# Optimization experiments

Measured on AMD Instinct MI355X. Metric: run time of the kernel, lower is better.

Reference implementation:

```python
import jax, jax.numpy as jnp
import numpy as np

B, L, D, DI, DS, DC, DTR = 128, 31, 1024, 2048, 16, 5, 64

def setup_inputs() -> dict:
    key = jax.random.key(0)
    ks = jax.random.split(key, 12)
    rn = lambda k, shp, s=0.02: jax.random.normal(k, shp, dtype=jnp.float32) * s
    return {
        "x": jax.random.normal(ks[0], (B, L, D), dtype=jnp.float32),
        "norm1_w": jnp.ones((D,), jnp.float32), "norm1_b": jnp.zeros((D,), jnp.float32),
        "in_proj_W": rn(ks[1], (2 * DI, D)),
        "conv_w": rn(ks[2], (DI, DC), 0.2), "conv_b": jnp.zeros((DI,), jnp.float32),
        "x_proj_W": rn(ks[3], (DTR + 2 * DS, DI)),
        "dt_proj_W": rn(ks[4], (DI, DTR), 0.1),
        "dt_proj_b": jnp.full((DI,), -4.6, dtype=jnp.float32),  # softplus^-1(~0.01)
        "A_log": jnp.tile(jnp.log(jnp.arange(1, DS + 1, dtype=jnp.float32))[None, :], (DI, 1)),
        "D_ssm": jnp.ones((DI,), jnp.float32),
        "out_proj_W": rn(ks[5], (D, DI)),
        "norm2_w": jnp.ones((D,), jnp.float32), "norm2_b": jnp.zeros((D,), jnp.float32),
        "ffn_W1": rn(ks[6], (2 * D, D)), "ffn_b1": jnp.zeros((2 * D,), jnp.float32),
        "ffn_W2": rn(ks[7], (D, 2 * D)), "ffn_b2": jnp.zeros((D,), jnp.float32),
        "cls_W1": rn(ks[8], (D, L * D)), "cls_b1": jnp.zeros((D,), jnp.float32),
        "cls_W2": rn(ks[9], (1, D)), "cls_b2": jnp.zeros((1,), jnp.float32),
    }

def _ln(x, w, b):
    m = x.mean(-1, keepdims=True)
    v = x.var(-1, keepdims=True)
    return (x - m) * jax.lax.rsqrt(v + 1e-5) * w + b

def _mamba(x, in_proj_W, conv_w, conv_b, x_proj_W, dt_proj_W, dt_proj_b, A_log, D_ssm, out_proj_W):
    # in_proj -> (u, z)
    xz = jnp.einsum('bld,ed->ble', x, in_proj_W)            # (B,L,2*DI)
    u, z = jnp.split(xz, 2, axis=-1)
    # causal depthwise conv1d (kernel DC) + SiLU
    xp = jnp.pad(u, ((0, 0), (DC - 1, 0), (0, 0)))
    uc = conv_b + sum(xp[:, k:k + L, :] * conv_w[:, k] for k in range(DC))
    uc = jax.nn.silu(uc)
    # input-dependent dt, B, C
    x_dbl = jnp.einsum('bld,ed->ble', uc, x_proj_W)         # (B,L,DTR+2*DS)
    dt, Bm, Cm = jnp.split(x_dbl, [DTR, DTR + DS], axis=-1)
    dt = jax.nn.softplus(jnp.einsum('blr,dr->bld', dt, dt_proj_W) + dt_proj_b)
    A = -jnp.exp(A_log)                                      # (DI,DS)
    def step(h, ins):
        dt_t, B_t, C_t, u_t = ins                            # (B,DI),(B,DS),(B,DS),(B,DI)
        dA = jnp.exp(dt_t[:, :, None] * A)                   # (B,DI,DS)
        h = h * dA + dt_t[:, :, None] * B_t[:, None, :] * u_t[:, :, None]
        y = jnp.einsum('bds,bs->bd', h, C_t)
        return h, y
    h0 = jnp.zeros((u.shape[0], DI, DS), u.dtype)
    _, ys = jax.lax.scan(step, h0, (dt.transpose(1, 0, 2), Bm.transpose(1, 0, 2),
                                    Cm.transpose(1, 0, 2), uc.transpose(1, 0, 2)))
    y = ys.transpose(1, 0, 2) + uc * D_ssm                   # skip term D*u
    y = y * jax.nn.silu(z)                                   # gate
    return jnp.einsum('bld,ed->ble', y, out_proj_W)

def reference(x, norm1_w, norm1_b, in_proj_W, conv_w, conv_b, x_proj_W, dt_proj_W,
              dt_proj_b, A_log, D_ssm, out_proj_W, norm2_w, norm2_b, ffn_W1, ffn_b1,
              ffn_W2, ffn_b2, cls_W1, cls_b1, cls_W2, cls_b2):
    # single encoder block (n_layers=1), dropout = identity (eval)
    res = x
    h = _ln(x, norm1_w, norm1_b)
    h = _mamba(h, in_proj_W, conv_w, conv_b, x_proj_W, dt_proj_W, dt_proj_b,
               A_log, D_ssm, out_proj_W)
    x = res + h
    res = x
    h = _ln(x, norm2_w, norm2_b)
    h = jax.nn.silu(jnp.einsum('bld,ed->ble', h, ffn_W1) + ffn_b1)
    h = jnp.einsum('ble,de->bld', h, ffn_W2) + ffn_b2
    x = res + h
    # classifier: Flatten -> Linear -> SiLU -> Linear
    flat = x.reshape(x.shape[0], -1)                          # (B, L*D)
    c = jax.nn.silu(flat @ cls_W1.T + cls_b1)
    out = c @ cls_W2.T + cls_b2                               # (B,1)
    return (out, x)
```

## Files before the change

### kernel.cpp

```cpp
#include <hip/hip_runtime.h>
#include <cstddef>
#include <cstdint>

#define B_   128
#define L_   31
#define D_   1024
#define DI_  2048
#define DS_  16
#define DC_  5
#define DTR_ 64
#define ROWS (B_ * L_)
#define MPAD 4096
#define KCLS (L_ * D_)

#define W_IN  0
#define W_OUT 4194304
#define W_F1  6291456
#define W_F2  8388608
#define W_XP  10485760
#define W_DT  10747904
#define WTOT  10878976

typedef unsigned short u16;
typedef __attribute__((ext_vector_type(8))) short s16x8;
typedef __attribute__((ext_vector_type(4))) float f32x4;

__device__ __forceinline__ float silu_f(float x) { return x / (1.0f + __expf(-x)); }

__device__ __forceinline__ u16 f2b(float f) {
    union { float f; uint32_t u; } c; c.f = f;
    uint32_t u = c.u + 0x7FFF + ((c.u >> 16) & 1);
    return (u16)(u >> 16);
}
__device__ __forceinline__ float b2f(u16 b) {
    union { uint32_t u; float f; } c; c.u = ((uint32_t)b) << 16;
    return c.f;
}
__device__ __forceinline__ uint32_t pack2(float lo, float hi) {
    return (uint32_t)f2b(lo) | ((uint32_t)f2b(hi) << 16);
}
__device__ __forceinline__ void cvt8(const float* __restrict__ s, u16* __restrict__ d) {
    const float4* p = (const float4*)s;
    float4 a = p[0], b = p[1];
    uint4 r;
    r.x = pack2(a.x, a.y); r.y = pack2(a.z, a.w);
    r.z = pack2(b.x, b.y); r.w = pack2(b.z, b.w);
    *(uint4*)d = r;
}

#define GLD16(g, s) __builtin_amdgcn_global_load_lds( \
    (const __attribute__((address_space(1))) void*)(g), \
    (__attribute__((address_space(3))) void*)(s), 16, 0, 0)

__global__ __launch_bounds__(256) void f2b_all_kernel(
    const float* __restrict__ inW, const float* __restrict__ outW,
    const float* __restrict__ f1W, const float* __restrict__ f2W,
    const float* __restrict__ xpW, const float* __restrict__ dtW,
    u16* __restrict__ wbuf)
{
    int g = blockIdx.x * 256 + threadIdx.x;
    if (g < 524288) { cvt8(inW + (size_t)g * 8, wbuf + W_IN + (size_t)g * 8); return; }
    g -= 524288;
    if (g < 262144) { cvt8(outW + (size_t)g * 8, wbuf + W_OUT + (size_t)g * 8); return; }
    g -= 262144;
    if (g < 262144) { cvt8(f1W + (size_t)g * 8, wbuf + W_F1 + (size_t)g * 8); return; }
    g -= 262144;
    if (g < 262144) { cvt8(f2W + (size_t)g * 8, wbuf + W_F2 + (size_t)g * 8); return; }
    g -= 262144;
    if (g < 32768) {
        const int row = g >> 8, col8 = (g & 255) * 8;
        u16* d = wbuf + W_XP + (size_t)row * 2048 + col8;
        if (row < 96) cvt8(xpW + (size_t)row * 2048 + col8, d);
        else *(uint4*)d = make_uint4(0, 0, 0, 0);
        return;
    }
    g -= 32768;
    if (g < 16384) cvt8(dtW + (size_t)g * 8, wbuf + W_DT + (size_t)g * 8);
}

__global__ __launch_bounds__(256) void ln_kernel(const float* __restrict__ x,
                                                 const float* __restrict__ w,
                                                 const float* __restrict__ b,
                                                 u16* __restrict__ y)
{
    const int row = blockIdx.x;
    const float* xr = x + (size_t)row * D_;
    float v[4];
    float sum = 0.f, sq = 0.f;
#pragma unroll
    for (int i = 0; i < 4; i++) {
        v[i] = xr[threadIdx.x + i * 256];
        sum += v[i];
        sq  += v[i] * v[i];
    }
#pragma unroll
    for (int o = 32; o > 0; o >>= 1) {
        sum += __shfl_down(sum, o, 64);
        sq  += __shfl_down(sq, o, 64);
    }
    __shared__ float red[8];
    const int wid = threadIdx.x >> 6;
    if ((threadIdx.x & 63) == 0) { red[wid] = sum; red[4 + wid] = sq; }
    __syncthreads();
    sum = red[0] + red[1] + red[2] + red[3];
    sq  = red[4] + red[5] + red[6] + red[7];
    const float mean = sum * (1.0f / D_);
    const float var  = sq * (1.0f / D_) - mean * mean;
    const float rstd = rsqrtf(var + 1e-5f);
    u16* yr = y + (size_t)row * D_;
#pragma unroll
    for (int i = 0; i < 4; i++) {
        const int c = threadIdx.x + i * 256;
        yr[c] = f2b((v[i] - mean) * rstd * w[c] + b[c]);
    }
}

__global__ __launch_bounds__(256) void ln2_fuse_kernel(const float* __restrict__ x,
                                                       const float* __restrict__ pq,
                                                       const float* __restrict__ w,
                                                       const float* __restrict__ b,
                                                       float* __restrict__ x2,
                                                       u16* __restrict__ y)
{
    const int row = blockIdx.x;
    const size_t base = (size_t)row * D_;
    const size_t PS = (size_t)ROWS * D_;
    float v[4];
    float sum = 0.f, sq = 0.f;
#pragma unroll
    for (int i = 0; i < 4; i++) {
        const int c = threadIdx.x + i * 256;
        float s = x[base + c];
        s += pq[base + c];
        s += pq[PS + base + c];
        s += pq[2 * PS + base + c];
        s += pq[3 * PS + base + c];
        x2[base + c] = s;
        v[i] = s;
        sum += s;
        sq  += s * s;
    }
#pragma unroll
    for (int o = 32; o > 0; o >>= 1) {
        sum += __shfl_down(sum, o, 64);
        sq  += __shfl_down(sq, o, 64);
    }
    __shared__ float red[8];
    const int wid = threadIdx.x >> 6;
    if ((threadIdx.x & 63) == 0) { red[wid] = sum; red[4 + wid] = sq; }
    __syncthreads();
    sum = red[0] + red[1] + red[2] + red[3];
    sq  = red[4] + red[5] + red[6] + red[7];
    const float mean = sum * (1.0f / D_);
    const float var  = sq * (1.0f / D_) - mean * mean;
    const float rstd = rsqrtf(var + 1e-5f);
    u16* yr = y + base;
#pragma unroll
    for (int i = 0; i < 4; i++) {
        const int c = threadIdx.x + i * 256;
        yr[c] = f2b((v[i] - mean) * rstd * w[c] + b[c]);
    }
}

__global__ __launch_bounds__(256) void add4_bias_kernel(const float* __restrict__ x2,
                                                        const float* __restrict__ pq,
                                                        const float* __restrict__ b2,
                                                        float* __restrict__ x3)
{
    const int i = blockIdx.x * 256 + threadIdx.x;
    const size_t PS4 = (size_t)ROWS * D_ / 4;
    float4 a  = ((const float4*)x2)[i];
    float4 c0 = ((const float4*)pq)[i];
    float4 c1 = ((const float4*)pq)[PS4 + i];
    float4 c2 = ((const float4*)pq)[2 * PS4 + i];
    float4 c3 = ((const float4*)pq)[3 * PS4 + i];
    float4 bb = ((const float4*)b2)[i & 255];
    float4 r;
    r.x = a.x + c0.x + c1.x + c2.x + c3.x + bb.x;
    r.y = a.y + c0.y + c1.y + c2.y + c3.y + bb.y;
    r.z = a.z + c0.z + c1.z + c2.z + c3.z + bb.z;
    r.w = a.w + c0.w + c1.w + c2.w + c3.w + bb.w;
    ((float4*)x3)[i] = r;
}

template <int ACT, bool BIAS, int OUT>
__global__ __launch_bounds__(512, 2) void gemm256(
    const u16* __restrict__ A, const u16* __restrict__ W,
    const float* __restrict__ bias, void* __restrict__ Cout,
    int K, int Nout, int kLen)
{
    __shared__ __align__(16) u16 As[2][256 * 64];
    __shared__ __align__(16) u16 Bs[2][256 * 64];
    const int tid = threadIdx.x;
    const int l = tid & 63;
    const int w = tid >> 6, wr = w >> 2, wc = w & 3;
    const int lane15 = l & 15, lhi = l >> 4;
    const int key = lane15 & 7;
    const int bm = blockIdx.y * 256, bn = blockIdx.x * 256;
    const int kOff = blockIdx.z * kLen;

    const int srow = tid >> 3;
    const int sg   = tid & 7;
    const int sgx  = sg ^ (srow & 7);
    const u16* gA = A + (size_t)(bm + srow) * K + kOff + sgx * 8;
    const u16* gB = W + (size_t)(bn + srow) * K + kOff + sgx * 8;
    const int soff = srow * 64 + sg * 8;

    const int NT = kLen / 64;
    f32x4 acc[8][4] = {};

#pragma unroll
    for (int c = 0; c < 4; c++) {
        GLD16(gA + (size_t)c * 64 * K, &As[0][c * 4096 + soff]);
        GLD16(gB + (size_t)c * 64 * K, &Bs[0][c * 4096 + soff]);
    }
    __syncthreads();

    for (int t = 0; t < NT; t++) {
        const int cur = t & 1;
        if (t + 1 < NT) {
            const size_t go = (size_t)(t + 1) * 64;
#pragma unroll
            for (int c = 0; c < 4; c++) {
                GLD16(gA + (size_t)c * 64 * K + go, &As[cur ^ 1][c * 4096 + soff]);
                GLD16(gB + (size_t)c * 64 * K + go, &Bs[cur ^ 1][c * 4096 + soff]);
            }
        }
        const u16* as = As[cur];
        const u16* bs = Bs[cur];
        s16x8 bf[2][4];
#pragma unroll
        for (int ks = 0; ks < 2; ks++)
#pragma unroll
            for (int ni = 0; ni < 4; ni++)
                bf[ks][ni] = *(const s16x8*)(bs + (wc * 64 + ni * 16 + lane15) * 64
                                                + (((ks * 4 + lhi) ^ key)) * 8);
#pragma unroll
        for (int mh = 0; mh < 2; mh++) {
            s16x8 af[2][4];
#pragma unroll
            for (int ks = 0; ks < 2; ks++)
#pragma unroll
                for (int mi = 0; mi < 4; mi++)
                    af[ks][mi] = *(const s16x8*)(as + (wr * 128 + mh * 64 + mi * 16 + lane15) * 64
                                                    + (((ks * 4 + lhi) ^ key)) * 8);
#pragma unroll
            for (int ks = 0; ks < 2; ks++)
#pragma unroll
                for (int mi = 0; mi < 4; mi++)
#pragma unroll
                    for (int ni = 0; ni < 4; ni++)
                        acc[mh * 4 + mi][ni] = __builtin_amdgcn_mfma_f32_16x16x32_bf16(
                            af[ks][mi], bf[ks][ni], acc[mh * 4 + mi][ni], 0, 0, 0);
        }
        __syncthreads();
    }

#pragma unroll
    for (int ni = 0; ni < 4; ni++) {
        const int col = bn + wc * 64 + ni * 16 + lane15;
        const float bv = BIAS ? bias[col] : 0.0f;
#pragma unroll
        for (int mi8 = 0; mi8 < 8; mi8++) {
#pragma unroll
            for (int r = 0; r < 4; r++) {
                const int row = bm + wr * 128 + mi8 * 16 + lhi * 4 + r;
                if (row >= ROWS) continue;
                float v = acc[mi8][ni][r] + bv;
                if (ACT == 1) v = silu_f(v);
                if (OUT == 1) ((u16*)Cout)[(size_t)row * Nout + col] = f2b(v);
                else          ((float*)Cout)[((size_t)blockIdx.z * ROWS + row) * Nout + col] = v;
            }
        }
    }
}

template <int ACT, bool BIAS, int OUT>
__global__ __launch_bounds__(256) void gemm_mfma(
    const u16* __restrict__ A, const u16* __restrict__ W,
    const float* __restrict__ bias, void* __restrict__ Cout,
    int M, int K, int Nout, int kLen)
{
    __shared__ __align__(16) u16 As[128 * 32];
    __shared__ __align__(16) u16 Bs[128 * 32];
    const int tid = threadIdx.x;
    const int l = tid & 63, w = tid >> 6;
    const int bm = blockIdx.y * 128, bn = blockIdx.x * 128;
    const int kOff = blockIdx.z * kLen;

    const int sr = l >> 2;
    const int sk = (l & 3) * 8;
    const u16* gA = A + (size_t)(bm + w * 16 + sr) * K + kOff + sk;
    const u16* gB = W + (size_t)(bn + w * 16 + sr) * K + kOff + sk;
    u16* lA = As + (w * 16 + sr) * 32 + sk;
    u16* lB = Bs + (w * 16 + sr) * 32 + sk;

    const int lane15 = l & 15, lhi = l >> 4;
    const int wr = w >> 1, wc = w & 1;
    const u16* fA = As + (wr * 64 + lane15) * 32 + lhi * 8;
    const u16* fB = Bs + (wc * 64 + lane15) * 32 + lhi * 8;

    f32x4 acc[4][4] = {};

    for (int kk = 0; kk < kLen; kk += 32) {
        GLD16(gA, lA); GLD16(gA + (size_t)64 * K, lA + 64 * 32);
        GLD16(gB, lB); GLD16(gB + (size_t)64 * K, lB + 64 * 32);
        gA += 32; gB += 32;
        __syncthreads();
        s16x8 af[4], bfr[4];
#pragma unroll
        for (int mi = 0; mi < 4; mi++) af[mi]  = *(const s16x8*)(fA + mi * 16 * 32);
#pragma unroll
        for (int ni = 0; ni < 4; ni++) bfr[ni] = *(const s16x8*)(fB + ni * 16 * 32);
#pragma unroll
        for (int mi = 0; mi < 4; mi++)
#pragma unroll
            for (int ni = 0; ni < 4; ni++)
                acc[mi][ni] = __builtin_amdgcn_mfma_f32_16x16x32_bf16(
                    af[mi], bfr[ni], acc[mi][ni], 0, 0, 0);
        __syncthreads();
    }

#pragma unroll
    for (int ni = 0; ni < 4; ni++) {
        const int col = bn + wc * 64 + ni * 16 + lane15;
        if (col >= Nout) continue;
        const float bv = BIAS ? bias[col] : 0.0f;
#pragma unroll
        for (int mi = 0; mi < 4; mi++) {
#pragma unroll
            for (int r = 0; r < 4; r++) {
                const int row = bm + wr * 64 + mi * 16 + lhi * 4 + r;
                float v = acc[mi][ni][r] + bv;
                if (ACT == 2) v = (v > 20.0f) ? v : log1pf(__expf(v));
                if (OUT == 1) ((u16*)Cout)[(size_t)row * Nout + col] = f2b(v);
                if (OUT == 2) atomicAdd(&((float*)Cout)[(size_t)row * Nout + col], v);
            }
        }
    }
}

#define KCH 512
__global__ __launch_bounds__(256) void gemm_cls_mfma(
    const float* __restrict__ A, const float* __restrict__ W,
    float* __restrict__ C)
{
    __shared__ __align__(16) u16 As[128 * 32];
    __shared__ __align__(16) u16 Bs[128 * 32];
    const int tid = threadIdx.x;
    const int l = tid & 63, w = tid >> 6;
    const int bn = blockIdx.x * 128;
    const int k0 = blockIdx.y * KCH;

    const int sr = l >> 2;
    const int sk = (l & 3) * 8;
    const int row = w * 16 + sr;
    const float* gA0 = A + (size_t)row * KCLS + k0 + sk;
    const float* gA1 = gA0 + (size_t)64 * KCLS;
    const float* gB0 = W + (size_t)(bn + row) * KCLS + k0 + sk;
    const float* gB1 = gB0 + (size_t)64 * KCLS;
    u16* lA0 = As + row * 32 + sk;  u16* lA1 = lA0 + 64 * 32;
    u16* lB0 = Bs + row * 32 + sk;  u16* lB1 = lB0 + 64 * 32;

    const int lane15 = l & 15, lhi = l >> 4;
    const int wr = w >> 1, wc = w & 1;
    const u16* fA = As + (wr * 64 + lane15) * 32 + lhi * 8;
    const u16* fB = Bs + (wc * 64 + lane15) * 32 + lhi * 8;

    f32x4 acc[4][4] = {};

    for (int ks = 0; ks < KCH / 32; ks++) {
        float4 a00 = *(const float4*)(gA0);     float4 a01 = *(const float4*)(gA0 + 4);
        float4 a10 = *(const float4*)(gA1);     float4 a11 = *(const float4*)(gA1 + 4);
        float4 b00 = *(const float4*)(gB0);     float4 b01 = *(const float4*)(gB0 + 4);
        float4 b10 = *(const float4*)(gB1);     float4 b11 = *(const float4*)(gB1 + 4);
        gA0 += 32; gA1 += 32; gB0 += 32; gB1 += 32;
        __syncthreads();
        uint4 r;
        r.x = pack2(a00.x, a00.y); r.y = pack2(a00.z, a00.w);
        r.z = pack2(a01.x, a01.y); r.w = pack2(a01.z, a01.w);
        *(uint4*)lA0 = r;
        r.x = pack2(a10.x, a10.y); r.y = pack2(a10.z, a10.w);
        r.z = pack2(a11.x, a11.y); r.w = pack2(a11.z, a11.w);
        *(uint4*)lA1 = r;
        r.x = pack2(b00.x, b00.y); r.y = pack2(b00.z, b00.w);
        r.z = pack2(b01.x, b01.y); r.w = pack2(b01.z, b01.w);
        *(uint4*)lB0 = r;
        r.x = pack2(b10.x, b10.y); r.y = pack2(b10.z, b10.w);
        r.z = pack2(b11.x, b11.y); r.w = pack2(b11.z, b11.w);
        *(uint4*)lB1 = r;
        __syncthreads();
        s16x8 af[4], bfr[4];
#pragma unroll
        for (int mi = 0; mi < 4; mi++) af[mi]  = *(const s16x8*)(fA + mi * 16 * 32);
#pragma unroll
        for (int ni = 0; ni < 4; ni++) bfr[ni] = *(const s16x8*)(fB + ni * 16 * 32);
#pragma unroll
        for (int mi = 0; mi < 4; mi++)
#pragma unroll
            for (int ni = 0; ni < 4; ni++)
                acc[mi][ni] = __builtin_amdgcn_mfma_f32_16x16x32_bf16(
                    af[mi], bfr[ni], acc[mi][ni], 0, 0, 0);
    }

#pragma unroll
    for (int ni = 0; ni < 4; ni++) {
        const int col = bn + wc * 64 + ni * 16 + lane15;
#pragma unroll
        for (int mi = 0; mi < 4; mi++) {
#pragma unroll
            for (int r = 0; r < 4; r++) {
                const int m = wr * 64 + mi * 16 + lhi * 4 + r;
                atomicAdd(&C[(size_t)m * 1024 + col], acc[mi][ni][r]);
            }
        }
    }
}

__global__ __launch_bounds__(256) void conv_silu_kernel(const u16* __restrict__ xz,
                                                        const float* __restrict__ cw,
                                                        const float* __restrict__ cb,
                                                        u16* __restrict__ uc)
{
    const int idx = blockIdx.x * 256 + threadIdx.x;
    const int d  = idx & (DI_ - 1);
    const int bl = idx >> 11;
    const int l  = bl % L_;
    const int b  = bl / L_;
    const u16* u = xz + (size_t)b * L_ * (2 * DI_) + d;
    float acc = cb[d];
#pragma unroll
    for (int k = 0; k < DC_; k++) {
        const int ll = l + k - (DC_ - 1);
        if (ll >= 0) acc = fmaf(b2f(u[(size_t)ll * (2 * DI_)]), cw[d * DC_ + k], acc);
    }
    uc[(size_t)bl * DI_ + d] = f2b(silu_f(acc));
}

__global__ __launch_bounds__(256) void dtext_kernel(const float* __restrict__ xdbl,
                                                    u16* __restrict__ dtb)
{
    const int idx = blockIdx.x * 256 + threadIdx.x;
    const int row = idx >> 4, c4 = (idx & 15) * 4;
    float4 v = *(const float4*)(xdbl + (size_t)row * 96 + c4);
    uint2 r;
    r.x = pack2(v.x, v.y); r.y = pack2(v.z, v.w);
    *(uint2*)(dtb + (size_t)row * 64 + c4) = r;
}

__global__ __launch_bounds__(256) void scan_kernel(const u16* __restrict__ dt,
                                                   const u16* __restrict__ uc,
                                                   const u16* __restrict__ xz,
                                                   const float* __restrict__ xdbl,
                                                   const float* __restrict__ A_log,
                                                   const float* __restrict__ D_ssm,
                                                   u16* __restrict__ y)
{
    const int idx = blockIdx.x * 256 + threadIdx.x;
    const int d = idx & (DI_ - 1);
    const int b = idx >> 11;
    float A[DS_];
#pragma unroll
    for (int s = 0; s < DS_; s++) A[s] = -__expf(A_log[d * DS_ + s]);
    const float Dv = D_ssm[d];
    float h[DS_] = {};
    for (int l = 0; l < L_; l++) {
        const size_t bl = (size_t)b * L_ + l;
        const float dtv = b2f(dt[bl * DI_ + d]);
        const float uv  = b2f(uc[bl * DI_ + d]);
        const float zv  = b2f(xz[bl * (2 * DI_) + DI_ + d]);
        const float* Bp = xdbl + bl * (DTR_ + 2 * DS_) + DTR_;
        const float* Cp = Bp + DS_;
        float yv = 0.f;
#pragma unroll
        for (int s = 0; s < DS_; s++) {
            h[s] = fmaf(h[s], __expf(dtv * A[s]), dtv * Bp[s] * uv);
            yv = fmaf(h[s], Cp[s], yv);
        }
        yv = fmaf(uv, Dv, yv);
        yv *= silu_f(zv);
        y[bl * DI_ + d] = f2b(yv);
    }
}

__global__ __launch_bounds__(256) void cls2_kernel(const float* __restrict__ c,
                                                   const float* __restrict__ b1,
                                                   const float* __restrict__ W2,
                                                   const float* __restrict__ b2,
                                                   float* __restrict__ out)
{
    const int b = blockIdx.x;
    float s = 0.f;
    for (int n = threadIdx.x; n < D_; n += 256) {
        float v = c[b * D_ + n] + b1[n];
        v = silu_f(v);
        s = fmaf(v, W2[n], s);
    }
#pragma unroll
    for (int o = 32; o > 0; o >>= 1) s += __shfl_down(s, o, 64);
    __shared__ float red[4];
    const int wid = threadIdx.x >> 6;
    if ((threadIdx.x & 63) == 0) red[wid] = s;
    __syncthreads();
    if (threadIdx.x == 0) out[b] = red[0] + red[1] + red[2] + red[3] + b2[0];
}

extern "C" void kernel_launch(void* const* d_in, const int* in_sizes, int n_in,
                              void* d_out, int out_size, void* d_ws, size_t ws_size,
                              hipStream_t stream)
{
    const float* x         = (const float*)d_in[0];
    const float* n1w       = (const float*)d_in[1];
    const float* n1b       = (const float*)d_in[2];
    const float* in_projW  = (const float*)d_in[3];
    const float* conv_w    = (const float*)d_in[4];
    const float* conv_b    = (const float*)d_in[5];
    const float* x_projW   = (const float*)d_in[6];
    const float* dt_projW  = (const float*)d_in[7];
    const float* dt_projb  = (const float*)d_in[8];
    const float* A_log     = (const float*)d_in[9];
    const float* D_ssm     = (const float*)d_in[10];
    const float* out_projW = (const float*)d_in[11];
    const float* n2w       = (const float*)d_in[12];
    const float* n2b       = (const float*)d_in[13];
    const float* ffn_W1    = (const float*)d_in[14];
    const float* ffn_b1    = (const float*)d_in[15];
    const float* ffn_W2    = (const float*)d_in[16];
    const float* ffn_b2    = (const float*)d_in[17];
    const float* cls_W1    = (const float*)d_in[18];
    const float* cls_b1    = (const float*)d_in[19];
    const float* cls_W2    = (const float*)d_in[20];
    const float* cls_b2    = (const float*)d_in[21];

    u16* base   = (u16*)d_ws;
    u16* xz_b   = base;
    u16* uc_b   = xz_b + (size_t)ROWS * 4096;
    u16* dt_b   = uc_b + (size_t)MPAD * 2048;
    u16* y_b    = dt_b + (size_t)ROWS * 2048;
    u16* h_b    = y_b + (size_t)MPAD * 2048;
    float* x2   = (float*)(h_b + (size_t)MPAD * 1024);
    float* xdbl = x2 + (size_t)ROWS * 1024;
    u16* dtb    = (u16*)(xdbl + (size_t)ROWS * 96);
    u16* wbuf   = dtb + (size_t)ROWS * 64;
    float* clsh = (float*)(wbuf + (size_t)WTOT);
    float* pq   = clsh + (size_t)B_ * D_;

    float* outv = (float*)d_out;
    float* x3   = outv + B_;

    f2b_all_kernel<<<dim3(5312), dim3(256), 0, stream>>>(
        in_projW, out_projW, ffn_W1, ffn_W2, x_projW, dt_projW, wbuf);
    ln_kernel<<<dim3(ROWS), dim3(256), 0, stream>>>(x, n1w, n1b, h_b);
    gemm256<0, false, 1><<<dim3(16, 16, 1), dim3(512), 0, stream>>>(
        h_b, wbuf + W_IN, nullptr, xz_b, D_, 2 * DI_, D_);
    conv_silu_kernel<<<dim3(ROWS * DI_ / 256), dim3(256), 0, stream>>>(xz_b, conv_w, conv_b, uc_b);
    hipMemsetAsync(xdbl, 0, (size_t)ROWS * 96 * sizeof(float), stream);
    gemm_mfma<0, false, 2><<<dim3(1, 31, 16), dim3(256), 0, stream>>>(
        uc_b, wbuf + W_XP, nullptr, xdbl, ROWS, DI_, DTR_ + 2 * DS_, 128);
    dtext_kernel<<<dim3(ROWS * 16 / 256), dim3(256), 0, stream>>>(xdbl, dtb);
    gemm_mfma<2, true, 1><<<dim3(16, 31, 1), dim3(256), 0, stream>>>(
        dtb, wbuf + W_DT, dt_projb, dt_b, ROWS, DTR_, DI_, DTR_);
    scan_kernel<<<dim3(B_ * DI_ / 256), dim3(256), 0, stream>>>(
        dt_b, uc_b, xz_b, xdbl, A_log, D_ssm, y_b);
    gemm256<0, false, 3><<<dim3(4, 16, 4), dim3(512), 0, stream>>>(
        y_b, wbuf + W_OUT, nullptr, pq, DI_, D_, 512);
    ln2_fuse_kernel<<<dim3(ROWS), dim3(256), 0, stream>>>(x, pq, n2w, n2b, x2, h_b);
    gemm256<1, true, 1><<<dim3(8, 16, 1), dim3(512), 0, stream>>>(
        h_b, wbuf + W_F1, ffn_b1, uc_b, D_, 2 * D_, D_);
    gemm256<0, false, 3><<<dim3(4, 16, 4), dim3(512), 0, stream>>>(
        uc_b, wbuf + W_F2, nullptr, pq, 2 * D_, D_, 512);
    add4_bias_kernel<<<dim3(ROWS * D_ / 4 / 256), dim3(256), 0, stream>>>(
        x2, pq, ffn_b2, x3);
    hipMemsetAsync(clsh, 0, (size_t)B_ * D_ * sizeof(float), stream);
    gemm_cls_mfma<<<dim3(1024 / 128, KCLS / KCH), dim3(256), 0, stream>>>(x3, cls_W1, clsh);
    cls2_kernel<<<dim3(B_), dim3(256), 0, stream>>>(clsh, cls_b1, cls_W2, cls_b2, outv);
}
```

Baseline: 442.8 us.

## Prefetch two K-tiles ahead with explicit vmcnt waits in 256x256 GEMM

Restructures the GEMM main loop so tiles t and t+1 are both issued before the loop. Each iteration waits with a partial vmcnt so only the current tile must have landed, and the tile t+2 load is issued into the just-freed buffer after the compute barrier. This keeps more global-to-LDS loads in flight to hide memory latency. It also raises wave priority around the MFMA block with s_setprio. The hardcoded vmcnt(8) depends on the exact count of outstanding loads per stage, and a mismatch would risk correctness.

```diff
diff --git a/kernel.cpp b/kernel.cpp
--- a/kernel.cpp
+++ b/kernel.cpp
@@ -209,23 +209,24 @@
     const int NT = kLen / 64;
     f32x4 acc[8][4] = {};
 
-#pragma unroll
-    for (int c = 0; c < 4; c++) {
-        GLD16(gA + (size_t)c * 64 * K, &As[0][c * 4096 + soff]);
-        GLD16(gB + (size_t)c * 64 * K, &Bs[0][c * 4096 + soff]);
-    }
-    __syncthreads();
+#define STAGE256(tt, bsel) do {                                             \
+    const size_t go_ = (size_t)(tt) * 64;                                   \
+    _Pragma("unroll")                                                       \
+    for (int c_ = 0; c_ < 4; c_++) {                                        \
+        GLD16(gA + (size_t)c_ * 64 * K + go_, &As[bsel][c_ * 4096 + soff]); \
+        GLD16(gB + (size_t)c_ * 64 * K + go_, &Bs[bsel][c_ * 4096 + soff]); \
+    }                                                                       \
+} while (0)
+
+    STAGE256(0, 0);
+    if (NT > 1) STAGE256(1, 1);
 
     for (int t = 0; t < NT; t++) {
         const int cur = t & 1;
-        if (t + 1 < NT) {
-            const size_t go = (size_t)(t + 1) * 64;
-#pragma unroll
-            for (int c = 0; c < 4; c++) {
-                GLD16(gA + (size_t)c * 64 * K + go, &As[cur ^ 1][c * 4096 + soff]);
-                GLD16(gB + (size_t)c * 64 * K + go, &Bs[cur ^ 1][c * 4096 + soff]);
-            }
-        }
+        if (t + 1 < NT) asm volatile("s_waitcnt vmcnt(8)" ::: "memory");
+        else            asm volatile("s_waitcnt vmcnt(0)" ::: "memory");
+        __builtin_amdgcn_s_barrier();
+
         const u16* as = As[cur];
         const u16* bs = Bs[cur];
         s16x8 bf[2][4];
@@ -235,6 +236,7 @@
             for (int ni = 0; ni < 4; ni++)
                 bf[ks][ni] = *(const s16x8*)(bs + (wc * 64 + ni * 16 + lane15) * 64
                                                 + (((ks * 4 + lhi) ^ key)) * 8);
+        __builtin_amdgcn_s_setprio(1);
 #pragma unroll
         for (int mh = 0; mh < 2; mh++) {
             s16x8 af[2][4];
@@ -253,8 +255,12 @@
                         acc[mh * 4 + mi][ni] = __builtin_amdgcn_mfma_f32_16x16x32_bf16(
                             af[ks][mi], bf[ks][ni], acc[mh * 4 + mi][ni], 0, 0, 0);
         }
-        __syncthreads();
-    }
+        __builtin_amdgcn_s_setprio(0);
+        asm volatile("s_waitcnt lgkmcnt(0)" ::: "memory");
+        __builtin_amdgcn_s_barrier();
+        if (t + 2 < NT) STAGE256(t + 2, cur);
+    }
+#undef STAGE256
 
 #pragma unroll
     for (int ni = 0; ni < 4; ni++) {
```

Result: no change. 443.9 us (+0.2%).
